# Kernel tuning notes

Measured on AMD Instinct MI355X. Metric: run time of the kernel, lower is better.

The kernel has to match this reference:

```python
import jax, jax.numpy as jnp
import numpy as np

D_MODEL = 1024
D_FFN = 4096
H = 16
D_HEAD = D_MODEL // H
B, L = 2, 2048
EPS = 1e-6


def layer_norm(x, a, b):
    # Matches torch: std is unbiased (ddof=1), and divides by (std + eps)
    mean = jnp.mean(x, axis=-1, keepdims=True)
    var = jnp.sum((x - mean) ** 2, axis=-1, keepdims=True) / (x.shape[-1] - 1)
    std = jnp.sqrt(var)
    return (x - mean) / (std + EPS) * a + b


def setup_inputs() -> dict:
    key = jax.random.key(0)
    ks = jax.random.split(key, 10)
    s = 0.02
    x = jax.random.normal(ks[0], (B, L, D_MODEL), dtype=jnp.float32)
    mask = jnp.tril(jnp.ones((L, L), dtype=jnp.int32))[None, None]  # causal [1,1,L,L]
    return {
        "x": x,
        "mask": mask,
        "Wqkv": jax.random.normal(ks[1], (D_MODEL, 3 * D_MODEL), jnp.float32) * s,
        "bqkv": jnp.zeros((3 * D_MODEL,), jnp.float32),
        "Wo": jax.random.normal(ks[2], (D_MODEL, D_MODEL), jnp.float32) * s,
        "bo": jnp.zeros((D_MODEL,), jnp.float32),
        "W1": jax.random.normal(ks[3], (D_MODEL, D_FFN), jnp.float32) * s,
        "b1": jnp.zeros((D_FFN,), jnp.float32),
        "W2": jax.random.normal(ks[4], (D_FFN, D_MODEL), jnp.float32) * s,
        "b2": jnp.zeros((D_MODEL,), jnp.float32),
        "ln1_a": jnp.ones((D_MODEL,), jnp.float32),
        "ln1_b": jnp.zeros((D_MODEL,), jnp.float32),
        "ln2_a": jnp.ones((D_MODEL,), jnp.float32),
        "ln2_b": jnp.zeros((D_MODEL,), jnp.float32),
    }


def reference(x, mask, Wqkv, bqkv, Wo, bo, W1, b1, W2, b2, ln1_a, ln1_b, ln2_a, ln2_b):
    b, l, d = x.shape
    # --- attention sublayer ---
    qkv = x @ Wqkv + bqkv                                   # [b, l, 3*d]
    qkv = qkv.reshape(b, l, 3, H, D_HEAD)                   # '(three h d)' ordering
    q, k, v = qkv[:, :, 0], qkv[:, :, 1], qkv[:, :, 2]      # each [b, l, h, dh]
    scores = jnp.einsum('bqhd,bkhd->bhqk', q, k) / jnp.sqrt(
        jnp.asarray(D_HEAD, x.dtype))                        # [b, h, lq, lk]
    scores = jnp.where(mask == 0, -jnp.inf, scores)
    p = jax.nn.softmax(scores, axis=-1)
    attn = jnp.einsum('bhqk,bkhd->bqhd', p, v).reshape(b, l, d)
    attn_out = attn @ Wo + bo
    x = layer_norm(x + attn_out, ln1_a, ln1_b)
    # --- MLP sublayer ---
    h = jax.nn.relu(x @ W1 + b1)
    mlp_out = h @ W2 + b2
    return layer_norm(x + mlp_out, ln2_a, ln2_b)
```

## Files before the change

kernel.cpp:

```cpp
#include <hip/hip_runtime.h>

#define D_MODEL 1024
#define D_FFN   4096
#define NH      16
#define DH      64
#define BB      2
#define LL      2048
#define MROWS   (BB * LL)

typedef unsigned short u16;
typedef unsigned int   u32;
typedef short bf16x8 __attribute__((ext_vector_type(8)));
typedef float f32x4  __attribute__((ext_vector_type(4)));

__device__ __forceinline__ float bf2f(u16 u) {
    union { u32 i; float f; } v;
    v.i = ((u32)u) << 16;
    return v.f;
}
__device__ __forceinline__ u16 f2bf(float f) {
    union { float f; u32 i; } v;
    v.f = f;
    u32 x = v.i;
    x += 0x7fffu + ((x >> 16) & 1u);
    return (u16)(x >> 16);
}
__device__ __forceinline__ u32 pack_bf_trunc(float a, float b) {
    return __builtin_amdgcn_perm(__float_as_uint(b), __float_as_uint(a),
                                 0x07060302u);
}

typedef const __attribute__((address_space(1))) u32 gu32;
typedef __attribute__((address_space(3))) u32 lu32;
__device__ __forceinline__ void gload_lds16(const void* g, void* l) {
    __builtin_amdgcn_global_load_lds((gu32*)g, (lu32*)l, 16, 0, 0);
}

__device__ __forceinline__ void wt_tile(
    const float* __restrict__ W, u16* __restrict__ Wt,
    int K, int N, int t, int tid, float* tile )
{
    const int ntiles = N >> 6;
    const int n0 = (t % ntiles) * 64;
    const int k0 = (t / ntiles) * 64;

    int kr = tid >> 4;
    int nc = (tid & 15) * 4;
    #pragma unroll
    for (int p = 0; p < 4; ++p) {
        float4 v = *(const float4*)&W[(size_t)(k0 + kr + p * 16) * N + n0 + nc];
        tile[(kr + p * 16) * 65 + nc + 0] = v.x;
        tile[(kr + p * 16) * 65 + nc + 1] = v.y;
        tile[(kr + p * 16) * 65 + nc + 2] = v.z;
        tile[(kr + p * 16) * 65 + nc + 3] = v.w;
    }
    __syncthreads();

    int nr = tid >> 2;
    int kc = (tid & 3) * 16;
    u16 o[16];
    #pragma unroll
    for (int j = 0; j < 16; ++j) o[j] = f2bf(tile[(kc + j) * 65 + nr]);
    u16* dst = &Wt[(size_t)(n0 + nr) * K + k0 + kc];
    *(uint4*)dst       = *(const uint4*)&o[0];
    *(uint4*)(dst + 8) = *(const uint4*)&o[8];
}

__global__ __launch_bounds__(256) void prep_kernel(
    const float* __restrict__ x,    u16* __restrict__ xb,
    const float* __restrict__ Wqkv, u16* __restrict__ Wqkvt)
{
    __shared__ float tile[64 * 65];
    const int tid = threadIdx.x;
    const int bi  = blockIdx.x;

    if (bi < 2048) {
        int i = bi * 2048 + tid * 8;
        float4 a = *(const float4*)(x + i);
        float4 b = *(const float4*)(x + i + 4);
        u16 o[8] = {f2bf(a.x), f2bf(a.y), f2bf(a.z), f2bf(a.w),
                    f2bf(b.x), f2bf(b.y), f2bf(b.z), f2bf(b.w)};
        *(uint4*)(xb + i) = *(const uint4*)o;
        return;
    }
    wt_tile(Wqkv, Wqkvt, 1024, 3072, bi - 2048, tid, tile);
}

template <int EPI, int RF32, int OF32, int KS>
__global__ __launch_bounds__(256, 4) void gemm_bt_kernel(
    const u16* __restrict__ A, const u16* __restrict__ Bt,
    const float* __restrict__ bias, const void* __restrict__ resv,
    void* __restrict__ out0v, u16* __restrict__ out1, u16* __restrict__ out2,
    int M, int N, int K)
{
    __shared__ u16 sA[128 * 64];
    __shared__ u16 sB[128 * 64];

    const int tid  = threadIdx.x;
    const int lane = tid & 63;
    const int wave = tid >> 6;
    const int wm   = (wave & 1) * 64;
    const int wn   = (wave >> 1) * 64;
    const int quad = lane >> 4;
    const int l16  = lane & 15;

    const int nb  = gridDim.x;
    const int mb  = gridDim.y;
    const int f   = blockIdx.y * nb + blockIdx.x;
    const int xcd = f & 7;
    const int idx = f >> 3;
    const int rn  = nb >> 1;
    const int rm  = mb >> 2;
    const int n0  = ((xcd & 1) * rn + (idx % rn)) * 128;
    const int ym  = (xcd >> 1) * rm + (idx / rn);

    int s, m0;
    if (KS > 1) {
        const int mt = mb / KS;
        s  = ym / mt;
        m0 = (ym % mt) * 128;
    } else {
        s  = 0;
        m0 = ym * 128;
    }
    const int Kseg = K / KS;
    const int kbeg = s * Kseg;

    f32x4 acc[4][4];
    #pragma unroll
    for (int i = 0; i < 4; ++i)
        #pragma unroll
        for (int j = 0; j < 4; ++j)
            acc[i][j] = (f32x4){0.f, 0.f, 0.f, 0.f};

    const u16* Ablk = A  + (size_t)m0 * K;
    const u16* Bblk = Bt + (size_t)n0 * K;

    for (int k0 = kbeg; k0 < kbeg + Kseg; k0 += 64) {
        #pragma unroll
        for (int i = 0; i < 4; ++i) {
            int chunk = (i * 4 + wave) * 64 + lane;
            int r = chunk >> 3;
            int c = (chunk & 7) ^ (r & 7);
            size_t goff = (size_t)r * K + k0 + c * 8;
            gload_lds16(Ablk + goff, &sA[(i * 4 + wave) * 512]);
            gload_lds16(Bblk + goff, &sB[(i * 4 + wave) * 512]);
        }
        __syncthreads();

        #pragma unroll
        for (int ks = 0; ks < 2; ++ks) {
            bf16x8 af[4], bfr[4];
            #pragma unroll
            for (int i = 0; i < 4; ++i) {
                int R = wm + i * 16 + l16;
                int slot = R * 8 + ((ks * 4 + quad) ^ (R & 7));
                af[i] = *(const bf16x8*)&sA[slot * 8];
            }
            #pragma unroll
            for (int j = 0; j < 4; ++j) {
                int R = wn + j * 16 + l16;
                int slot = R * 8 + ((ks * 4 + quad) ^ (R & 7));
                bfr[j] = *(const bf16x8*)&sB[slot * 8];
            }
            #pragma unroll
            for (int i = 0; i < 4; ++i)
                #pragma unroll
                for (int j = 0; j < 4; ++j)
                    acc[i][j] = __builtin_amdgcn_mfma_f32_16x16x32_bf16(
                        af[i], bfr[j], acc[i][j], 0, 0, 0);
        }
        __syncthreads();
    }

    #pragma unroll
    for (int i = 0; i < 4; ++i) {
        int rowb = m0 + wm + i * 16 + quad * 4;
        #pragma unroll
        for (int j = 0; j < 4; ++j) {
            int col = n0 + wn + j * 16 + l16;
            float bv = (EPI == 3) ? 0.f : bias[col];
            #pragma unroll
            for (int r = 0; r < 4; ++r) {
                int rr = rowb + r;
                float v = acc[i][j][r] + bv;
                if (EPI == 0) {
                    int which = col >> 10;
                    int h     = (col >> 6) & 15;
                    int d     = col & 63;
                    int b     = rr >> 11;
                    int l     = rr & 2047;
                    size_t idx2 = ((size_t)(b * NH + h) * LL + l) * DH + d;
                    u16* o0 = (u16*)out0v;
                    if (which == 0)      o0[idx2]   = f2bf(v * 0.18033688f);
                    else if (which == 1) out1[idx2] = f2bf(v);
                    else                 out2[idx2] = f2bf(v);
                } else if (EPI == 3) {
                    ((u16*)out0v)[((size_t)s * M + rr) * N + col] = f2bf(v);
                } else {
                    size_t idx2 = (size_t)rr * N + col;
                    if (EPI == 1) {
                        v += RF32 ? ((const float*)resv)[idx2]
                                  : bf2f(((const u16*)resv)[idx2]);
                    } else {
                        v = v > 0.f ? v : 0.f;
                    }
                    if (OF32) ((float*)out0v)[idx2] = v;
                    else      ((u16*)out0v)[idx2]   = f2bf(v);
                }
            }
        }
    }
}

template <int KS, int RF32, int OF32>
__global__ __launch_bounds__(256) void lnfuse_kernel(
    const u16* __restrict__ P, const float* __restrict__ bias,
    const void* __restrict__ resv,
    const float* __restrict__ ga, const float* __restrict__ gb,
    void* __restrict__ outv)
{
    __shared__ float red[8];
    const int tid  = threadIdx.x;
    const int lane = tid & 63;
    const int wave = tid >> 6;
    const size_t row = blockIdx.x;
    const size_t SL  = (size_t)MROWS * D_MODEL;
    const int c = tid * 4;

    float v0, v1, v2, v3;
    {
        float4 bv = *(const float4*)(bias + c);
        v0 = bv.x; v1 = bv.y; v2 = bv.z; v3 = bv.w;
    }
    #pragma unroll
    for (int s = 0; s < KS; ++s) {
        uint2 p = *(const uint2*)(P + s * SL + row * D_MODEL + c);
        v0 += bf2f((u16)p.x); v1 += bf2f((u16)(p.x >> 16));
        v2 += bf2f((u16)p.y); v3 += bf2f((u16)(p.y >> 16));
    }
    if (RF32) {
        float4 r = *(const float4*)((const float*)resv + row * D_MODEL + c);
        v0 += r.x; v1 += r.y; v2 += r.z; v3 += r.w;
    } else {
        uint2 r = *(const uint2*)((const u16*)resv + row * D_MODEL + c);
        v0 += bf2f((u16)r.x); v1 += bf2f((u16)(r.x >> 16));
        v2 += bf2f((u16)r.y); v3 += bf2f((u16)(r.y >> 16));
    }

    float s_ = v0 + v1 + v2 + v3;
    #pragma unroll
    for (int o = 32; o > 0; o >>= 1) s_ += __shfl_xor(s_, o, 64);
    if (lane == 0) red[wave] = s_;
    __syncthreads();
    float mean = (red[0] + red[1] + red[2] + red[3]) * (1.f / 1024.f);

    float d0 = v0 - mean, d1 = v1 - mean, d2 = v2 - mean, d3 = v3 - mean;
    float q = d0 * d0 + d1 * d1 + d2 * d2 + d3 * d3;
    #pragma unroll
    for (int o = 32; o > 0; o >>= 1) q += __shfl_xor(q, o, 64);
    if (lane == 0) red[4 + wave] = q;
    __syncthreads();
    float var = (red[4] + red[5] + red[6] + red[7]) * (1.f / 1023.f);
    float inv = 1.f / (sqrtf(var) + 1e-6f);

    float y0 = d0 * inv * ga[c + 0] + gb[c + 0];
    float y1 = d1 * inv * ga[c + 1] + gb[c + 1];
    float y2 = d2 * inv * ga[c + 2] + gb[c + 2];
    float y3 = d3 * inv * ga[c + 3] + gb[c + 3];
    if (OF32) {
        float4 y = {y0, y1, y2, y3};
        *(float4*)((float*)outv + row * D_MODEL + c) = y;
    } else {
        ushort4 y = {f2bf(y0), f2bf(y1), f2bf(y2), f2bf(y3)};
        *(ushort4*)((u16*)outv + row * D_MODEL + c) = y;
    }
}

__global__ __launch_bounds__(256) void attn_kernel(
    const u16* __restrict__ Q, const u16* __restrict__ K,
    const u16* __restrict__ V, u16* __restrict__ out,
    const float* __restrict__ Wo, u16* __restrict__ Wot,
    const float* __restrict__ W1, u16* __restrict__ W1t,
    const float* __restrict__ W2, u16* __restrict__ W2t)
{
    __shared__ u16 smem[18432];
    u16* ks = smem;
    u16* vs = smem + 4608;
    u16* ps = smem + 9216;

    const int tid  = threadIdx.x;
    const int bi   = blockIdx.x;

    if (bi >= 512) {
        float* tile = (float*)smem;
        int t = bi - 512;
        if (t < 256)       wt_tile(Wo, Wot, 1024, 1024, t,        tid, tile);
        else if (t < 1280) wt_tile(W1, W1t, 1024, 4096, t - 256,  tid, tile);
        else               wt_tile(W2, W2t, 4096, 1024, t - 1280, tid, tile);
        return;
    }

    const int lane = tid & 63;
    const int wave = tid >> 6;
    const int l16  = lane & 15;
    const int quad = lane >> 4;

    const int f   = bi;
    const int xcd = f & 7;
    const int idx = f >> 3;
    const int bh  = xcd * 4 + (idx >> 4);
    const int pr  = idx & 15;
    const int b   = bh >> 4, h = bh & 15;
    const size_t head_off = (size_t)bh * LL * DH;

    const u16* Qh = Q + head_off;
    const u16* Kh = K + head_off;
    const u16* Vh = V + head_off;

    const int qtA = 31 - pr, qtB = pr;
    const int baseA = qtA * 64 + wave * 16;
    const int baseB = qtB * 64 + wave * 16;
    const int qgA   = baseA + l16;
    const int qgB   = baseB + l16;

    const bf16x8 qfA0 = *(const bf16x8*)&Qh[(size_t)qgA * DH + quad * 8];
    const bf16x8 qfA1 = *(const bf16x8*)&Qh[(size_t)qgA * DH + 32 + quad * 8];
    const bf16x8 qfB0 = *(const bf16x8*)&Qh[(size_t)qgB * DH + quad * 8];
    const bf16x8 qfB1 = *(const bf16x8*)&Qh[(size_t)qgB * DH + 32 + quad * 8];

    float lA = 0.f, lB = 0.f;
    f32x4 oA[4], oB[4];
    #pragma unroll
    for (int t = 0; t < 4; ++t) {
        oA[t] = (f32x4){0.f, 0.f, 0.f, 0.f};
        oB[t] = (f32x4){0.f, 0.f, 0.f, 0.f};
    }

    u16* psA = ps + wave * 2304;
    u16* psB = psA + 1152;

    const int key = tid >> 2;
    const int kd0 = (tid & 3) * 16;
    const int kp  = tid >> 3;
    const int vd0 = (tid & 7) * 8;

    uint4 kr0, kr1, vr0, vr1;
    {
        const u16* ksrc = Kh + (size_t)key * DH + kd0;
        kr0 = *(const uint4*)ksrc;
        kr1 = *(const uint4*)(ksrc + 8);
        const u16* vsrc = Vh + (size_t)(2 * kp) * DH + vd0;
        vr0 = *(const uint4*)vsrc;
        vr1 = *(const uint4*)(vsrc + DH);
    }

    for (int c = 0; c <= qtA; ++c) {
        const bool doB = (c <= qtB);
        __syncthreads();
        *(uint4*)&ks[key * 72 + kd0]     = kr0;
        *(uint4*)&ks[key * 72 + kd0 + 8] = kr1;
        {
            const u32* w0 = (const u32*)&vr0;
            const u32* w1 = (const u32*)&vr1;
            #pragma unroll
            for (int e = 0; e < 8; ++e) {
                int d = vd0 + e;
                u32 lo = (w0[e >> 1] >> ((e & 1) * 16)) & 0xffffu;
                u32 hi = (w1[e >> 1] >> ((e & 1) * 16)) & 0xffffu;
                int csw = kp ^ (4 * ((d >> 3) & 7));
                *(u32*)&vs[d * 72 + 2 * csw] = lo | (hi << 16);
            }
        }
        __syncthreads();
        if (c < qtA) {
            const u16* ksrc = Kh + (size_t)((c + 1) * 64 + key) * DH + kd0;
            kr0 = *(const uint4*)ksrc;
            kr1 = *(const uint4*)(ksrc + 8);
            const u16* vsrc = Vh + (size_t)((c + 1) * 64 + 2 * kp) * DH + vd0;
            vr0 = *(const uint4*)vsrc;
            vr1 = *(const uint4*)(vsrc + DH);
        }

        f32x4 stA[4], stB[4];
        #pragma unroll
        for (int t = 0; t < 4; ++t) {
            bf16x8 k0 = *(const bf16x8*)&ks[(t * 16 + l16) * 72 + quad * 8];
            bf16x8 k1 = *(const bf16x8*)&ks[(t * 16 + l16) * 72 + 32 + quad * 8];
            f32x4 s = (f32x4){0.f, 0.f, 0.f, 0.f};
            s = __builtin_amdgcn_mfma_f32_16x16x32_bf16(k0, qfA0, s, 0, 0, 0);
            s = __builtin_amdgcn_mfma_f32_16x16x32_bf16(k1, qfA1, s, 0, 0, 0);
            stA[t] = s;
            if (doB) {
                f32x4 s2 = (f32x4){0.f, 0.f, 0.f, 0.f};
                s2 = __builtin_amdgcn_mfma_f32_16x16x32_bf16(k0, qfB0, s2, 0, 0, 0);
                s2 = __builtin_amdgcn_mfma_f32_16x16x32_bf16(k1, qfB1, s2, 0, 0, 0);
                stB[t] = s2;
            }
        }

        if (c == qtA) {
            #pragma unroll
            for (int t = 0; t < 4; ++t)
                #pragma unroll
                for (int r = 0; r < 4; ++r)
                    if (c * 64 + t * 16 + quad * 4 + r > qgA) stA[t][r] = -INFINITY;
        }
        if (doB && c == qtB) {
            #pragma unroll
            for (int t = 0; t < 4; ++t)
                #pragma unroll
                for (int r = 0; r < 4; ++r)
                    if (c * 64 + t * 16 + quad * 4 + r > qgB) stB[t][r] = -INFINITY;
        }

        {
            float psum = 0.f;
            #pragma unroll
            for (int t = 0; t < 4; ++t) {
                float p0 = exp2f(stA[t][0]), p1 = exp2f(stA[t][1]);
                float p2 = exp2f(stA[t][2]), p3 = exp2f(stA[t][3]);
                psum += (p0 + p1) + (p2 + p3);
                uint2 w = {pack_bf_trunc(p0, p1), pack_bf_trunc(p2, p3)};
                *(uint2*)&psA[l16 * 72 + t * 16 + quad * 4] = w;
            }
            psum += __shfl_xor(psum, 16, 64);
            psum += __shfl_xor(psum, 32, 64);
            lA += psum;
        }
        if (doB) {
            float psum = 0.f;
            #pragma unroll
            for (int t = 0; t < 4; ++t) {
                float p0 = exp2f(stB[t][0]), p1 = exp2f(stB[t][1]);
                float p2 = exp2f(stB[t][2]), p3 = exp2f(stB[t][3]);
                psum += (p0 + p1) + (p2 + p3);
                uint2 w = {pack_bf_trunc(p0, p1), pack_bf_trunc(p2, p3)};
                *(uint2*)&psB[l16 * 72 + t * 16 + quad * 4] = w;
            }
            psum += __shfl_xor(psum, 16, 64);
            psum += __shfl_xor(psum, 32, 64);
            lB += psum;
        }

        bf16x8 pfA0 = *(const bf16x8*)&psA[l16 * 72 + quad * 8];
        bf16x8 pfA1 = *(const bf16x8*)&psA[l16 * 72 + 32 + quad * 8];
        bf16x8 pfB0, pfB1;
        if (doB) {
            pfB0 = *(const bf16x8*)&psB[l16 * 72 + quad * 8];
            pfB1 = *(const bf16x8*)&psB[l16 * 72 + 32 + quad * 8];
        }

        #pragma unroll
        for (int dt = 0; dt < 4; ++dt) {
            int d  = dt * 16 + l16;
            int sw = 4 * ((d >> 3) & 7);
            bf16x8 vf0 = *(const bf16x8*)&vs[d * 72 + 2 * ((quad * 4) ^ sw)];
            bf16x8 vf1 = *(const bf16x8*)&vs[d * 72 + 2 * ((16 + quad * 4) ^ sw)];
            oA[dt] = __builtin_amdgcn_mfma_f32_16x16x32_bf16(pfA0, vf0, oA[dt], 0, 0, 0);
            oA[dt] = __builtin_amdgcn_mfma_f32_16x16x32_bf16(pfA1, vf1, oA[dt], 0, 0, 0);
            if (doB) {
                oB[dt] = __builtin_amdgcn_mfma_f32_16x16x32_bf16(pfB0, vf0, oB[dt], 0, 0, 0);
                oB[dt] = __builtin_amdgcn_mfma_f32_16x16x32_bf16(pfB1, vf1, oB[dt], 0, 0, 0);
            }
        }
    }

    {
        float i0 = 1.f / __shfl(lA, quad * 4 + 0, 64);
        float i1 = 1.f / __shfl(lA, quad * 4 + 1, 64);
        float i2 = 1.f / __shfl(lA, quad * 4 + 2, 64);
        float i3 = 1.f / __shfl(lA, quad * 4 + 3, 64);
        #pragma unroll
        for (int dt = 0; dt < 4; ++dt) {
            size_t col = h * DH + dt * 16 + l16;
            size_t r0  = ((size_t)b * LL + baseA + quad * 4) * D_MODEL + col;
            out[r0]               = f2bf(oA[dt][0] * i0);
            out[r0 + D_MODEL]     = f2bf(oA[dt][1] * i1);
            out[r0 + 2 * D_MODEL] = f2bf(oA[dt][2] * i2);
            out[r0 + 3 * D_MODEL] = f2bf(oA[dt][3] * i3);
        }
    }
    {
        float i0 = 1.f / __shfl(lB, quad * 4 + 0, 64);
        float i1 = 1.f / __shfl(lB, quad * 4 + 1, 64);
        float i2 = 1.f / __shfl(lB, quad * 4 + 2, 64);
        float i3 = 1.f / __shfl(lB, quad * 4 + 3, 64);
        #pragma unroll
        for (int dt = 0; dt < 4; ++dt) {
            size_t col = h * DH + dt * 16 + l16;
            size_t r0  = ((size_t)b * LL + baseB + quad * 4) * D_MODEL + col;
            out[r0]               = f2bf(oB[dt][0] * i0);
            out[r0 + D_MODEL]     = f2bf(oB[dt][1] * i1);
            out[r0 + 2 * D_MODEL] = f2bf(oB[dt][2] * i2);
            out[r0 + 3 * D_MODEL] = f2bf(oB[dt][3] * i3);
        }
    }
}

extern "C" void kernel_launch(void* const* d_in, const int* in_sizes, int n_in,
                              void* d_out, int out_size, void* d_ws, size_t ws_size,
                              hipStream_t stream)
{
    const float* x    = (const float*)d_in[0];
    const float* Wqkv = (const float*)d_in[2];
    const float* bqkv = (const float*)d_in[3];
    const float* Wo   = (const float*)d_in[4];
    const float* bo   = (const float*)d_in[5];
    const float* W1   = (const float*)d_in[6];
    const float* b1   = (const float*)d_in[7];
    const float* W2   = (const float*)d_in[8];
    const float* b2   = (const float*)d_in[9];
    const float* ln1a = (const float*)d_in[10];
    const float* ln1b = (const float*)d_in[11];
    const float* ln2a = (const float*)d_in[12];
    const float* ln2b = (const float*)d_in[13];

    char* ws = (char*)d_ws;
    const size_t HSZ = (size_t)BB * NH * LL * DH;
    u16*   Qp    = (u16*)ws;
    u16*   Kp    = Qp + HSZ;
    u16*   Vp    = Kp + HSZ;
    u16*   attn  = Vp + HSZ;
    u16*   hbuf  = (u16*)ws;
    u16*   xb    = (u16*)(ws + 33554432);
    u16*   x1    = (u16*)(ws + 50331648);
    u16*   Wqkvt = (u16*)(ws + 58720256);
    u16*   Wot   = (u16*)(ws + 65011712);
    u16*   W1t   = (u16*)(ws + 67108864);
    u16*   W2t   = (u16*)(ws + 75497472);
    u16*   Pbuf  = (u16*)(ws + 83886080);

    dim3 blk(256);

    prep_kernel<<<dim3(2816), blk, 0, stream>>>(x, xb, Wqkv, Wqkvt);

    gemm_bt_kernel<0,0,0,1><<<dim3(24, 32), blk, 0, stream>>>(
        xb, Wqkvt, bqkv, nullptr, Qp, Kp, Vp, MROWS, 3 * D_MODEL, D_MODEL);
    attn_kernel<<<dim3(2816), blk, 0, stream>>>(
        Qp, Kp, Vp, attn, Wo, Wot, W1, W1t, W2, W2t);
    gemm_bt_kernel<3,0,0,2><<<dim3(8, 64), blk, 0, stream>>>(
        attn, Wot, bo, nullptr, Pbuf, nullptr, nullptr, MROWS, D_MODEL, D_MODEL);
    lnfuse_kernel<2,1,0><<<dim3(MROWS), blk, 0, stream>>>(
        Pbuf, bo, x, ln1a, ln1b, x1);
    gemm_bt_kernel<2,0,0,1><<<dim3(32, 32), blk, 0, stream>>>(
        x1, W1t, b1, nullptr, hbuf, nullptr, nullptr, MROWS, D_FFN, D_MODEL);
    gemm_bt_kernel<3,0,0,4><<<dim3(8, 128), blk, 0, stream>>>(
        hbuf, W2t, b2, nullptr, Pbuf, nullptr, nullptr, MROWS, D_MODEL, D_FFN);
    lnfuse_kernel<4,0,1><<<dim3(MROWS), blk, 0, stream>>>(
        Pbuf, b2, x1, ln2a, ln2b, d_out);
}
```

Baseline: 314.8 us.

## Split paired causal query tiles into separate attention blocks

Each attention block used to process two query tiles (a long and a short one) so that causal work was balanced per block. Now each block handles a single 64-row query tile, which doubles the attention block count to 1024 and orders blocks longest-first. LDS use per block drops, which allows more blocks per CU and reduces register pressure from the dual accumulators. In exchange, K/V tiles are loaded once per query tile instead of being shared by two, and per-block work becomes uneven, so the result depends on the scheduler balancing the load.

```diff
diff --git a/kernel.cpp b/kernel.cpp
--- a/kernel.cpp
+++ b/kernel.cpp
@@ -284,7 +284,7 @@
     const float* __restrict__ W1, u16* __restrict__ W1t,
     const float* __restrict__ W2, u16* __restrict__ W2t)
 {
-    __shared__ u16 smem[18432];
+    __shared__ u16 smem[13824];
     u16* ks = smem;
     u16* vs = smem + 4608;
     u16* ps = smem + 9216;
@@ -292,9 +292,9 @@
     const int tid  = threadIdx.x;
     const int bi   = blockIdx.x;
 
-    if (bi >= 512) {
+    if (bi >= 1024) {
         float* tile = (float*)smem;
-        int t = bi - 512;
+        int t = bi - 1024;
         if (t < 256)       wt_tile(Wo, Wot, 1024, 1024, t,        tid, tile);
         else if (t < 1280) wt_tile(W1, W1t, 1024, 4096, t - 256,  tid, tile);
         else               wt_tile(W2, W2t, 4096, 1024, t - 1280, tid, tile);
@@ -306,11 +306,10 @@
     const int l16  = lane & 15;
     const int quad = lane >> 4;
 
-    const int f   = bi;
-    const int xcd = f & 7;
-    const int idx = f >> 3;
-    const int bh  = xcd * 4 + (idx >> 4);
-    const int pr  = idx & 15;
+    const int xcd = bi & 7;
+    const int idx = bi >> 3;
+    const int bh  = xcd * 4 + (idx & 3);
+    const int qt  = 31 - (idx >> 2);
     const int b   = bh >> 4, h = bh & 15;
     const size_t head_off = (size_t)bh * LL * DH;
 
@@ -318,27 +317,18 @@
     const u16* Kh = K + head_off;
     const u16* Vh = V + head_off;
 
-    const int qtA = 31 - pr, qtB = pr;
-    const int baseA = qtA * 64 + wave * 16;
-    const int baseB = qtB * 64 + wave * 16;
-    const int qgA   = baseA + l16;
-    const int qgB   = baseB + l16;
-
-    const bf16x8 qfA0 = *(const bf16x8*)&Qh[(size_t)qgA * DH + quad * 8];
-    const bf16x8 qfA1 = *(const bf16x8*)&Qh[(size_t)qgA * DH + 32 + quad * 8];
-    const bf16x8 qfB0 = *(const bf16x8*)&Qh[(size_t)qgB * DH + quad * 8];
-    const bf16x8 qfB1 = *(const bf16x8*)&Qh[(size_t)qgB * DH + 32 + quad * 8];
-
-    float lA = 0.f, lB = 0.f;
-    f32x4 oA[4], oB[4];
-    #pragma unroll
-    for (int t = 0; t < 4; ++t) {
-        oA[t] = (f32x4){0.f, 0.f, 0.f, 0.f};
-        oB[t] = (f32x4){0.f, 0.f, 0.f, 0.f};
-    }
-
-    u16* psA = ps + wave * 2304;
-    u16* psB = psA + 1152;
+    const int base = qt * 64 + wave * 16;
+    const int qg   = base + l16;
+
+    const bf16x8 qf0 = *(const bf16x8*)&Qh[(size_t)qg * DH + quad * 8];
+    const bf16x8 qf1 = *(const bf16x8*)&Qh[(size_t)qg * DH + 32 + quad * 8];
+
+    float lsum = 0.f;
+    f32x4 o[4];
+    #pragma unroll
+    for (int t = 0; t < 4; ++t) o[t] = (f32x4){0.f, 0.f, 0.f, 0.f};
+
+    u16* psw = ps + wave * 1152;
 
     const int key = tid >> 2;
     const int kd0 = (tid & 3) * 16;
@@ -355,8 +345,7 @@
         vr1 = *(const uint4*)(vsrc + DH);
     }
 
-    for (int c = 0; c <= qtA; ++c) {
-        const bool doB = (c <= qtB);
+    for (int c = 0; c <= qt; ++c) {
         __syncthreads();
         *(uint4*)&ks[key * 72 + kd0]     = kr0;
         *(uint4*)&ks[key * 72 + kd0 + 8] = kr1;
@@ -373,7 +362,7 @@
             }
         }
         __syncthreads();
-        if (c < qtA) {
+        if (c < qt) {
             const u16* ksrc = Kh + (size_t)((c + 1) * 64 + key) * DH + kd0;
             kr0 = *(const uint4*)ksrc;
             kr1 = *(const uint4*)(ksrc + 8);
@@ -382,74 +371,42 @@
             vr1 = *(const uint4*)(vsrc + DH);
         }
 
-        f32x4 stA[4], stB[4];
+        f32x4 st[4];
         #pragma unroll
         for (int t = 0; t < 4; ++t) {
             bf16x8 k0 = *(const bf16x8*)&ks[(t * 16 + l16) * 72 + quad * 8];
             bf16x8 k1 = *(const bf16x8*)&ks[(t * 16 + l16) * 72 + 32 + quad * 8];
             f32x4 s = (f32x4){0.f, 0.f, 0.f, 0.f};
-            s = __builtin_amdgcn_mfma_f32_16x16x32_bf16(k0, qfA0, s, 0, 0, 0);
-            s = __builtin_amdgcn_mfma_f32_16x16x32_bf16(k1, qfA1, s, 0, 0, 0);
-            stA[t] = s;
-            if (doB) {
-                f32x4 s2 = (f32x4){0.f, 0.f, 0.f, 0.f};
-                s2 = __builtin_amdgcn_mfma_f32_16x16x32_bf16(k0, qfB0, s2, 0, 0, 0);
-                s2 = __builtin_amdgcn_mfma_f32_16x16x32_bf16(k1, qfB1, s2, 0, 0, 0);
-                stB[t] = s2;
-            }
-        }
-
-        if (c == qtA) {
+            s = __builtin_amdgcn_mfma_f32_16x16x32_bf16(k0, qf0, s, 0, 0, 0);
+            s = __builtin_amdgcn_mfma_f32_16x16x32_bf16(k1, qf1, s, 0, 0, 0);
+            st[t] = s;
+        }
+
+        if (c == qt) {
             #pragma unroll
             for (int t = 0; t < 4; ++t)
                 #pragma unroll
                 for (int r = 0; r < 4; ++r)
-                    if (c * 64 + t * 16 + quad * 4 + r > qgA) stA[t][r] = -INFINITY;
-        }
-        if (doB && c == qtB) {
-            #pragma unroll
-            for (int t = 0; t < 4; ++t)
-                #pragma unroll
-                for (int r = 0; r < 4; ++r)
-                    if (c * 64 + t * 16 + quad * 4 + r > qgB) stB[t][r] = -INFINITY;
+                    if (c * 64 + t * 16 + quad * 4 + r > qg) st[t][r] = -INFINITY;
         }
 
         {
             float psum = 0.f;
             #pragma unroll
             for (int t = 0; t < 4; ++t) {
-                float p0 = exp2f(stA[t][0]), p1 = exp2f(stA[t][1]);
-                float p2 = exp2f(stA[t][2]), p3 = exp2f(stA[t][3]);
+                float p0 = exp2f(st[t][0]), p1 = exp2f(st[t][1]);
+                float p2 = exp2f(st[t][2]), p3 = exp2f(st[t][3]);
                 psum += (p0 + p1) + (p2 + p3);
                 uint2 w = {pack_bf_trunc(p0, p1), pack_bf_trunc(p2, p3)};
-                *(uint2*)&psA[l16 * 72 + t * 16 + quad * 4] = w;
+                *(uint2*)&psw[l16 * 72 + t * 16 + quad * 4] = w;
             }
             psum += __shfl_xor(psum, 16, 64);
             psum += __shfl_xor(psum, 32, 64);
-            lA += psum;
-        }
-        if (doB) {
-            float psum = 0.f;
-            #pragma unroll
-            for (int t = 0; t < 4; ++t) {
-                float p0 = exp2f(stB[t][0]), p1 = exp2f(stB[t][1]);
-                float p2 = exp2f(stB[t][2]), p3 = exp2f(stB[t][3]);
-                psum += (p0 + p1) + (p2 + p3);
-                uint2 w = {pack_bf_trunc(p0, p1), pack_bf_trunc(p2, p3)};
-                *(uint2*)&psB[l16 * 72 + t * 16 + quad * 4] = w;
-            }
-            psum += __shfl_xor(psum, 16, 64);
-            psum += __shfl_xor(psum, 32, 64);
-            lB += psum;
-        }
-
-        bf16x8 pfA0 = *(const bf16x8*)&psA[l16 * 72 + quad * 8];
-        bf16x8 pfA1 = *(const bf16x8*)&psA[l16 * 72 + 32 + quad * 8];
-        bf16x8 pfB0, pfB1;
-        if (doB) {
-            pfB0 = *(const bf16x8*)&psB[l16 * 72 + quad * 8];
-            pfB1 = *(const bf16x8*)&psB[l16 * 72 + 32 + quad * 8];
-        }
+            lsum += psum;
+        }
+
+        bf16x8 pf0 = *(const bf16x8*)&psw[l16 * 72 + quad * 8];
+        bf16x8 pf1 = *(const bf16x8*)&psw[l16 * 72 + 32 + quad * 8];
 
         #pragma unroll
         for (int dt = 0; dt < 4; ++dt) {
@@ -457,43 +414,24 @@
             int sw = 4 * ((d >> 3) & 7);
             bf16x8 vf0 = *(const bf16x8*)&vs[d * 72 + 2 * ((quad * 4) ^ sw)];
             bf16x8 vf1 = *(const bf16x8*)&vs[d * 72 + 2 * ((16 + quad * 4) ^ sw)];
-            oA[dt] = __builtin_amdgcn_mfma_f32_16x16x32_bf16(pfA0, vf0, oA[dt], 0, 0, 0);
-            oA[dt] = __builtin_amdgcn_mfma_f32_16x16x32_bf16(pfA1, vf1, oA[dt], 0, 0, 0);
-            if (doB) {
-                oB[dt] = __builtin_amdgcn_mfma_f32_16x16x32_bf16(pfB0, vf0, oB[dt], 0, 0, 0);
-                oB[dt] = __builtin_amdgcn_mfma_f32_16x16x32_bf16(pfB1, vf1, oB[dt], 0, 0, 0);
-            }
+            o[dt] = __builtin_amdgcn_mfma_f32_16x16x32_bf16(pf0, vf0, o[dt], 0, 0, 0);
+            o[dt] = __builtin_amdgcn_mfma_f32_16x16x32_bf16(pf1, vf1, o[dt], 0, 0, 0);
         }
     }
 
     {
-        float i0 = 1.f / __shfl(lA, quad * 4 + 0, 64);
-        float i1 = 1.f / __shfl(lA, quad * 4 + 1, 64);
-        float i2 = 1.f / __shfl(lA, quad * 4 + 2, 64);
-        float i3 = 1.f / __shfl(lA, quad * 4 + 3, 64);
+        float i0 = 1.f / __shfl(lsum, quad * 4 + 0, 64);
+        float i1 = 1.f / __shfl(lsum, quad * 4 + 1, 64);
+        float i2 = 1.f / __shfl(lsum, quad * 4 + 2, 64);
+        float i3 = 1.f / __shfl(lsum, quad * 4 + 3, 64);
         #pragma unroll
         for (int dt = 0; dt < 4; ++dt) {
             size_t col = h * DH + dt * 16 + l16;
-            size_t r0  = ((size_t)b * LL + baseA + quad * 4) * D_MODEL + col;
-            out[r0]               = f2bf(oA[dt][0] * i0);
-            out[r0 + D_MODEL]     = f2bf(oA[dt][1] * i1);
-            out[r0 + 2 * D_MODEL] = f2bf(oA[dt][2] * i2);
-            out[r0 + 3 * D_MODEL] = f2bf(oA[dt][3] * i3);
-        }
-    }
-    {
-        float i0 = 1.f / __shfl(lB, quad * 4 + 0, 64);
-        float i1 = 1.f / __shfl(lB, quad * 4 + 1, 64);
-        float i2 = 1.f / __shfl(lB, quad * 4 + 2, 64);
-        float i3 = 1.f / __shfl(lB, quad * 4 + 3, 64);
-        #pragma unroll
-        for (int dt = 0; dt < 4; ++dt) {
-            size_t col = h * DH + dt * 16 + l16;
-            size_t r0  = ((size_t)b * LL + baseB + quad * 4) * D_MODEL + col;
-            out[r0]               = f2bf(oB[dt][0] * i0);
-            out[r0 + D_MODEL]     = f2bf(oB[dt][1] * i1);
-            out[r0 + 2 * D_MODEL] = f2bf(oB[dt][2] * i2);
-            out[r0 + 3 * D_MODEL] = f2bf(oB[dt][3] * i3);
+            size_t r0  = ((size_t)b * LL + base + quad * 4) * D_MODEL + col;
+            out[r0]               = f2bf(o[dt][0] * i0);
+            out[r0 + D_MODEL]     = f2bf(o[dt][1] * i1);
+            out[r0 + 2 * D_MODEL] = f2bf(o[dt][2] * i2);
+            out[r0 + 3 * D_MODEL] = f2bf(o[dt][3] * i3);
         }
     }
 }
@@ -537,7 +475,7 @@
 
     gemm_bt_kernel<0,0,0,1><<<dim3(24, 32), blk, 0, stream>>>(
         xb, Wqkvt, bqkv, nullptr, Qp, Kp, Vp, MROWS, 3 * D_MODEL, D_MODEL);
-    attn_kernel<<<dim3(2816), blk, 0, stream>>>(
+    attn_kernel<<<dim3(3328), blk, 0, stream>>>(
         Qp, Kp, Vp, attn, Wo, Wot, W1, W1t, W2, W2t);
     gemm_bt_kernel<3,0,0,2><<<dim3(8, 64), blk, 0, stream>>>(
         attn, Wot, bo, nullptr, Pbuf, nullptr, nullptr, MROWS, D_MODEL, D_MODEL);
```

Result: no change. 319.1 us (+1.4%).
